# Performance work log

Measured on AMD Instinct MI355X. Metric: run time of the kernel, lower is better.

Reference implementation:

```python
import jax, jax.numpy as jnp
import numpy as np

B, C, H, W, R = 4, 128, 64, 256, 8  # batch, channels, height, width, window radius


def setup_inputs() -> dict:
    key = jax.random.key(0)
    k0, k1, k2, k3 = jax.random.split(key, 4)
    feature = jax.random.normal(k0, (B, C, H, W), dtype=jnp.float32)
    position = 0.02 * jax.random.normal(k1, (B, C, H, W), dtype=jnp.float32)
    # 1x1 conv weights (xavier-like scale), bias zeros as in nn.Conv2d default-ish
    Wq = jax.random.normal(k2, (C, C), dtype=jnp.float32) / np.float32(np.sqrt(C))
    Wk = jax.random.normal(k3, (C, C), dtype=jnp.float32) / np.float32(np.sqrt(C))
    bq = jnp.zeros((C,), dtype=jnp.float32)
    bk = jnp.zeros((C,), dtype=jnp.float32)
    return {"feature": feature, "position": position, "Wq": Wq, "bq": bq, "Wk": Wk, "bk": bk}


def reference(feature, position, Wq, bq, Wk, bk):
    # feature/position: [b, c, h, w]
    f = feature + position
    b, c, h, w = f.shape
    # 1x1 convs == channel matmuls
    q = jnp.einsum('oc,bchw->bohw', Wq, f) + bq[None, :, None, None]
    k = jnp.einsum('oc,bchw->bohw', Wk, f) + bk[None, :, None, None]
    r = R
    Kw = 2 * r + 1
    # pad along width, gather sliding windows: [b, c, h, w, Kw]
    kp = jnp.pad(k, ((0, 0), (0, 0), (0, 0), (r, r)))
    vp = jnp.pad(f, ((0, 0), (0, 0), (0, 0), (r, r)))
    idx = jnp.arange(w)[:, None] + jnp.arange(Kw)[None, :]  # [w, Kw]
    kwin = kp[:, :, :, idx]
    vwin = vp[:, :, :, idx]
    scale = jnp.asarray(np.sqrt(c), dtype=q.dtype)
    scores = jnp.einsum('bchw,bchwk->bhwk', q, kwin) / scale  # [b, h, w, Kw]
    attn = jax.nn.softmax(scores, axis=-1)
    out = jnp.einsum('bhwk,bchwk->bchw', attn, vwin)
    return out
```

## Files before the change

### kernel.cpp

```cpp
#include <hip/hip_runtime.h>
#include <hip/hip_bf16.h>
#include <math.h>

#define BB 4
#define CCH 128
#define HH 64
#define WW 256
#define RR 8
#define KWIN 17
#define TW 32
#define TWH 48
#define NTHREADS 256
#define PIT 136
#define PTP 56
#define MROWS 144

typedef __attribute__((ext_vector_type(8))) short short8;
typedef __attribute__((ext_vector_type(4))) short short4v;
typedef __attribute__((ext_vector_type(4))) float f32x4;

__device__ __forceinline__ short f2bf(float x) {
    union { __hip_bfloat16 b; short s; } u;
    u.b = __float2bfloat16(x);
    return u.s;
}

__global__ __launch_bounds__(256)
void prep_kernel(const float* __restrict__ Wq, const float* __restrict__ bq,
                 const float* __restrict__ Wk, short* __restrict__ Mp)
{
    const int t = threadIdx.x;
    const int r = blockIdx.x * 2 + (t >> 7);
    const int c = t & 127;
    float a0 = 0.f, a1 = 0.f, a2 = 0.f, a3 = 0.f;
    if (r < CCH) {
        #pragma unroll
        for (int j = 0; j < CCH; j += 4) {
            a0 = fmaf(Wq[(j + 0) * CCH + r], Wk[(j + 0) * CCH + c], a0);
            a1 = fmaf(Wq[(j + 1) * CCH + r], Wk[(j + 1) * CCH + c], a1);
            a2 = fmaf(Wq[(j + 2) * CCH + r], Wk[(j + 2) * CCH + c], a2);
            a3 = fmaf(Wq[(j + 3) * CCH + r], Wk[(j + 3) * CCH + c], a3);
        }
    } else if (r == CCH) {
        #pragma unroll
        for (int o = 0; o < CCH; o += 4) {
            a0 = fmaf(bq[o + 0], Wk[(o + 0) * CCH + c], a0);
            a1 = fmaf(bq[o + 1], Wk[(o + 1) * CCH + c], a1);
            a2 = fmaf(bq[o + 2], Wk[(o + 2) * CCH + c], a2);
            a3 = fmaf(bq[o + 3], Wk[(o + 3) * CCH + c], a3);
        }
    }
    Mp[r * CCH + c] = f2bf((a0 + a1) + (a2 + a3));
}

#define ST_IDX(r) (((r) >> 4) * 1088 + ((r) & 15) * 36)

__global__ __launch_bounds__(NTHREADS, 5)
void attn1d_fused(const float* __restrict__ feature,
                  const float* __restrict__ position,
                  const short* __restrict__ Mp,
                  float* __restrict__ out)
{
    __shared__ __align__(16) short fBt[TWH][PIT];
    __shared__ __align__(16) char  uB[TWH * PIT * 2];
    __shared__ __align__(16) short Pt[TW][PTP];
    __shared__ float ubias[TWH];
    short (*gT)[PIT]  = (short(*)[PIT])uB;
    float* Stp        = (float*)uB;

    const int t    = threadIdx.x;
    const int wid  = t >> 6;
    const int lane = t & 63;
    const int lrow = lane & 15;
    const int lgrp = lane >> 4;

    int blk = blockIdx.x;
    blk = (blk & 7) * 256 + (blk >> 3);
    const int wt = blk & 7;
    const int bh = blk >> 3;
    const int h  = bh & (HH - 1);
    const int b  = bh >> 6;
    const int w0 = wt * TW - RR;
    const int base = ((b * CCH) * HH + h) * WW;

    const int mrow = wid * 32;
    short8 Mf[2][4];
    #pragma unroll
    for (int mf = 0; mf < 2; ++mf)
        #pragma unroll
        for (int kk = 0; kk < 4; ++kk)
            Mf[mf][kk] = *(const short8*)(Mp + (mrow + mf * 16 + lrow) * CCH
                                             + kk * 32 + lgrp * 8);
    short8 Mf2[4];
    if (wid == 3) {
        #pragma unroll
        for (int kk = 0; kk < 4; ++kk)
            Mf2[kk] = *(const short8*)(Mp + (CCH + lrow) * CCH + kk * 32 + lgrp * 8);
    }

    #pragma unroll
    for (int i = 0; i < 6; ++i) {
        const int idx = i * NTHREADS + t;
        const int c  = idx / 12;
        const int wq = idx - c * 12;
        const int w  = w0 + wq * 4;
        float4 fv = {0.f, 0.f, 0.f, 0.f};
        if (w >= 0 && w < WW) {
            const int off = base + c * (HH * WW) + w;
            const float4 fa = *(const float4*)(feature + off);
            const float4 pa = *(const float4*)(position + off);
            fv.x = fa.x + pa.x; fv.y = fa.y + pa.y;
            fv.z = fa.z + pa.z; fv.w = fa.w + pa.w;
        }
        fBt[wq * 4 + 0][c] = f2bf(fv.x);
        fBt[wq * 4 + 1][c] = f2bf(fv.y);
        fBt[wq * 4 + 2][c] = f2bf(fv.z);
        fBt[wq * 4 + 3][c] = f2bf(fv.w);
    }
    __syncthreads();

    {
        f32x4 acc[2][3];
        #pragma unroll
        for (int mf = 0; mf < 2; ++mf)
            #pragma unroll
            for (int nf = 0; nf < 3; ++nf)
                acc[mf][nf] = (f32x4){0.f, 0.f, 0.f, 0.f};
        f32x4 acc2[3];
        #pragma unroll
        for (int nf = 0; nf < 3; ++nf) acc2[nf] = (f32x4){0.f, 0.f, 0.f, 0.f};

        #pragma unroll
        for (int kk = 0; kk < 4; ++kk) {
            short8 bfr[3];
            #pragma unroll
            for (int nf = 0; nf < 3; ++nf)
                bfr[nf] = *(const short8*)&fBt[nf * 16 + lrow][kk * 32 + lgrp * 8];
            #pragma unroll
            for (int mf = 0; mf < 2; ++mf)
                #pragma unroll
                for (int nf = 0; nf < 3; ++nf)
                    acc[mf][nf] = __builtin_amdgcn_mfma_f32_16x16x32_bf16(
                        Mf[mf][kk], bfr[nf], acc[mf][nf], 0, 0, 0);
            if (wid == 3) {
                #pragma unroll
                for (int nf = 0; nf < 3; ++nf)
                    acc2[nf] = __builtin_amdgcn_mfma_f32_16x16x32_bf16(
                        Mf2[kk], bfr[nf], acc2[nf], 0, 0, 0);
            }
        }

        #pragma unroll
        for (int mf = 0; mf < 2; ++mf)
            #pragma unroll
            for (int nf = 0; nf < 3; ++nf) {
                short4v s;
                #pragma unroll
                for (int reg = 0; reg < 4; ++reg)
                    s[reg] = f2bf(acc[mf][nf][reg]);
                *(short4v*)&gT[nf * 16 + lrow][mrow + mf * 16 + lgrp * 4] = s;
            }
        if (wid == 3 && lgrp == 0) {
            const float isc = 0.08838834764831845f;
            #pragma unroll
            for (int nf = 0; nf < 3; ++nf)
                ubias[nf * 16 + lrow] = acc2[nf][0] * isc;
        }
    }
    __syncthreads();

    if (wid < 3) {
        const int nf = wid;
        f32x4 s0 = {0.f,0.f,0.f,0.f}, s1 = {0.f,0.f,0.f,0.f};
        #pragma unroll
        for (int kk = 0; kk < 4; ++kk) {
            const short8 a0 = *(const short8*)&fBt[RR + lrow     ][kk * 32 + lgrp * 8];
            const short8 a1 = *(const short8*)&fBt[RR + 16 + lrow][kk * 32 + lgrp * 8];
            const short8 bb = *(const short8*)&gT[nf * 16 + lrow][kk * 32 + lgrp * 8];
            s0 = __builtin_amdgcn_mfma_f32_16x16x32_bf16(a0, bb, s0, 0, 0, 0);
            s1 = __builtin_amdgcn_mfma_f32_16x16x32_bf16(a1, bb, s1, 0, 0, 0);
        }
        const float isc = 0.08838834764831845f;
        const int sb = ST_IDX(nf * 16 + lrow);
        *(f32x4*)&Stp[sb + lgrp * 4]      = s0 * isc;
        *(f32x4*)&Stp[sb + 16 + lgrp * 4] = s1 * isc;
    } else {
        const short8 z = {0,0,0,0,0,0,0,0};
        short* p = &Pt[0][0];
        #pragma unroll
        for (int i = 0; i < 4; ++i) {
            const int q8 = i * 64 + lane;
            if (q8 < (TW * PTP) / 8) *(short8*)(p + q8 * 8) = z;
        }
    }
    __syncthreads();

    if (t < TW * 4) {
        const int w = t >> 2, g = t & 3;
        const int nt = (g == 0) ? 5 : 4;
        float sv[5];
        float mx = -3.0e38f;
        #pragma unroll
        for (int i = 0; i < 5; ++i) {
            if (i < nt) {
                const int j = (i == 4) ? 16 : (g + i * 4);
                const int r = w + j;
                sv[i] = Stp[ST_IDX(r) + w] + ubias[r];
                mx = fmaxf(mx, sv[i]);
            }
        }
        mx = fmaxf(mx, __shfl_xor(mx, 1, 4));
        mx = fmaxf(mx, __shfl_xor(mx, 2, 4));
        float sum = 0.f;
        #pragma unroll
        for (int i = 0; i < 5; ++i)
            if (i < nt) { sv[i] = __expf(sv[i] - mx); sum += sv[i]; }
        sum += __shfl_xor(sum, 1, 4);
        sum += __shfl_xor(sum, 2, 4);
        const float inv = 1.f / sum;
        #pragma unroll
        for (int i = 0; i < 5; ++i)
            if (i < nt) {
                const int j = (i == 4) ? 16 : (g + i * 4);
                Pt[w][w + j] = f2bf(sv[i] * inv);
            }
    }
    __syncthreads();

    {
        const int cb = wid * 32;
        const short8 z = {0,0,0,0,0,0,0,0};
        f32x4 d00 = {0.f,0.f,0.f,0.f}, d01 = d00, d10 = d00, d11 = d00;
        #pragma unroll
        for (int kk = 0; kk < 2; ++kk) {
            const int koff = kk * 32 + lgrp * 8;
            const bool live = (koff < TWH);
            short8 a0 = z, a1 = z, b0 = z, b1 = z;
            if (live) {
                #pragma unroll
                for (int j = 0; j < 8; ++j) {
                    a0[j] = fBt[koff + j][cb + lrow];
                    a1[j] = fBt[koff + j][cb + 16 + lrow];
                }
                b0 = *(const short8*)&Pt[lrow][koff];
                b1 = *(const short8*)&Pt[16 + lrow][koff];
            }
            d00 = __builtin_amdgcn_mfma_f32_16x16x32_bf16(a0, b0, d00, 0, 0, 0);
            d01 = __builtin_amdgcn_mfma_f32_16x16x32_bf16(a0, b1, d01, 0, 0, 0);
            d10 = __builtin_amdgcn_mfma_f32_16x16x32_bf16(a1, b0, d10, 0, 0, 0);
            d11 = __builtin_amdgcn_mfma_f32_16x16x32_bf16(a1, b1, d11, 0, 0, 0);
        }
        const int wbase = wt * TW;
        #pragma unroll
        for (int reg = 0; reg < 4; ++reg) {
            const int c0 = cb + lgrp * 4 + reg;
            out[base + c0 * (HH * WW)        + wbase + lrow]      = d00[reg];
            out[base + c0 * (HH * WW)        + wbase + 16 + lrow] = d01[reg];
            out[base + (c0 + 16) * (HH * WW) + wbase + lrow]      = d10[reg];
            out[base + (c0 + 16) * (HH * WW) + wbase + 16 + lrow] = d11[reg];
        }
    }
}

extern "C" void kernel_launch(void* const* d_in, const int* in_sizes, int n_in,
                              void* d_out, int out_size, void* d_ws, size_t ws_size,
                              hipStream_t stream) {
    const float* feature  = (const float*)d_in[0];
    const float* position = (const float*)d_in[1];
    const float* Wq = (const float*)d_in[2];
    const float* bq = (const float*)d_in[3];
    const float* Wk = (const float*)d_in[4];
    const float* bk = (const float*)d_in[5];
    (void)bk;
    float* out = (float*)d_out;
    short* Mp  = (short*)d_ws;

    prep_kernel<<<MROWS / 2, 256, 0, stream>>>(Wq, bq, Wk, Mp);
    const dim3 grid(BB * HH * (WW / TW));
    attn1d_fused<<<grid, NTHREADS, 0, stream>>>(feature, position, Mp, out);
}
```

Measured before the change: 43.36 us.

## Widen attention tile to 64 columns with 512 threads and channel-major value copy

Doubles the width tile from 32 to 64 output columns per block, so the 16-column halo is amortized over more outputs. Threads go from 256 to 512 and work is repartitioned across 8 waves. It also adds a channel-major bf16 copy of the features so the final P·V MFMA can read its A operand with vector loads instead of strided scalar gathers. In exchange, shared memory per block grows (a separate score/gT buffer plus the new fA array), which lowers occupancy, and there are half as many blocks.

```diff
diff --git a/kernel.cpp b/kernel.cpp
--- a/kernel.cpp
+++ b/kernel.cpp
@@ -8,11 +8,12 @@
 #define WW 256
 #define RR 8
 #define KWIN 17
-#define TW 32
-#define TWH 48
-#define NTHREADS 256
+#define TW 64
+#define TWH 80
+#define NTHREADS 512
 #define PIT 136
-#define PTP 56
+#define FAP 88
+#define PTP 88
 #define MROWS 144
 
 typedef __attribute__((ext_vector_type(8))) short short8;
@@ -53,20 +54,18 @@
     Mp[r * CCH + c] = f2bf((a0 + a1) + (a2 + a3));
 }
 
-#define ST_IDX(r) (((r) >> 4) * 1088 + ((r) & 15) * 36)
-
-__global__ __launch_bounds__(NTHREADS, 5)
+__global__ __launch_bounds__(NTHREADS, 4)
 void attn1d_fused(const float* __restrict__ feature,
                   const float* __restrict__ position,
                   const short* __restrict__ Mp,
                   float* __restrict__ out)
 {
     __shared__ __align__(16) short fBt[TWH][PIT];
-    __shared__ __align__(16) char  uB[TWH * PIT * 2];
-    __shared__ __align__(16) short Pt[TW][PTP];
+    __shared__ __align__(16) short gT [TWH][PIT];
+    __shared__ __align__(16) short fA [CCH][FAP];
+    __shared__ __align__(16) short Pt [TW ][PTP];
     __shared__ float ubias[TWH];
-    short (*gT)[PIT]  = (short(*)[PIT])uB;
-    float* Stp        = (float*)uB;
+    float* Stp = (float*)&gT[0][0];
 
     const int t    = threadIdx.x;
     const int wid  = t >> 6;
@@ -75,34 +74,31 @@
     const int lgrp = lane >> 4;
 
     int blk = blockIdx.x;
-    blk = (blk & 7) * 256 + (blk >> 3);
-    const int wt = blk & 7;
-    const int bh = blk >> 3;
+    blk = (blk & 7) * 128 + (blk >> 3);
+    const int wt = blk & 3;
+    const int bh = blk >> 2;
     const int h  = bh & (HH - 1);
     const int b  = bh >> 6;
     const int w0 = wt * TW - RR;
     const int base = ((b * CCH) * HH + h) * WW;
 
-    const int mrow = wid * 32;
-    short8 Mf[2][4];
+    const int mrow = wid * 16;
+    short8 Mf[4];
     #pragma unroll
-    for (int mf = 0; mf < 2; ++mf)
-        #pragma unroll
-        for (int kk = 0; kk < 4; ++kk)
-            Mf[mf][kk] = *(const short8*)(Mp + (mrow + mf * 16 + lrow) * CCH
-                                             + kk * 32 + lgrp * 8);
+    for (int kk = 0; kk < 4; ++kk)
+        Mf[kk] = *(const short8*)(Mp + (mrow + lrow) * CCH + kk * 32 + lgrp * 8);
     short8 Mf2[4];
-    if (wid == 3) {
+    if (wid == 7) {
         #pragma unroll
         for (int kk = 0; kk < 4; ++kk)
             Mf2[kk] = *(const short8*)(Mp + (CCH + lrow) * CCH + kk * 32 + lgrp * 8);
     }
 
     #pragma unroll
-    for (int i = 0; i < 6; ++i) {
+    for (int i = 0; i < 5; ++i) {
         const int idx = i * NTHREADS + t;
-        const int c  = idx / 12;
-        const int wq = idx - c * 12;
+        const int c  = idx / 20;
+        const int wq = idx - c * 20;
         const int w  = w0 + wq * 4;
         float4 fv = {0.f, 0.f, 0.f, 0.f};
         if (w >= 0 && w < WW) {
@@ -112,153 +108,151 @@
             fv.x = fa.x + pa.x; fv.y = fa.y + pa.y;
             fv.z = fa.z + pa.z; fv.w = fa.w + pa.w;
         }
-        fBt[wq * 4 + 0][c] = f2bf(fv.x);
-        fBt[wq * 4 + 1][c] = f2bf(fv.y);
-        fBt[wq * 4 + 2][c] = f2bf(fv.z);
-        fBt[wq * 4 + 3][c] = f2bf(fv.w);
+        short4v s4;
+        s4[0] = f2bf(fv.x); s4[1] = f2bf(fv.y); s4[2] = f2bf(fv.z); s4[3] = f2bf(fv.w);
+        *(short4v*)&fA[c][wq * 4] = s4;
+        fBt[wq * 4 + 0][c] = s4[0];
+        fBt[wq * 4 + 1][c] = s4[1];
+        fBt[wq * 4 + 2][c] = s4[2];
+        fBt[wq * 4 + 3][c] = s4[3];
     }
     __syncthreads();
 
     {
-        f32x4 acc[2][3];
-        #pragma unroll
-        for (int mf = 0; mf < 2; ++mf)
-            #pragma unroll
-            for (int nf = 0; nf < 3; ++nf)
-                acc[mf][nf] = (f32x4){0.f, 0.f, 0.f, 0.f};
-        f32x4 acc2[3];
-        #pragma unroll
-        for (int nf = 0; nf < 3; ++nf) acc2[nf] = (f32x4){0.f, 0.f, 0.f, 0.f};
+        f32x4 acc[5];
+        #pragma unroll
+        for (int nf = 0; nf < 5; ++nf) acc[nf] = (f32x4){0.f, 0.f, 0.f, 0.f};
+        f32x4 acc2[5];
+        #pragma unroll
+        for (int nf = 0; nf < 5; ++nf) acc2[nf] = (f32x4){0.f, 0.f, 0.f, 0.f};
 
         #pragma unroll
         for (int kk = 0; kk < 4; ++kk) {
-            short8 bfr[3];
-            #pragma unroll
-            for (int nf = 0; nf < 3; ++nf)
+            short8 bfr[5];
+            #pragma unroll
+            for (int nf = 0; nf < 5; ++nf)
                 bfr[nf] = *(const short8*)&fBt[nf * 16 + lrow][kk * 32 + lgrp * 8];
             #pragma unroll
-            for (int mf = 0; mf < 2; ++mf)
+            for (int nf = 0; nf < 5; ++nf)
+                acc[nf] = __builtin_amdgcn_mfma_f32_16x16x32_bf16(
+                    Mf[kk], bfr[nf], acc[nf], 0, 0, 0);
+            if (wid == 7) {
                 #pragma unroll
-                for (int nf = 0; nf < 3; ++nf)
-                    acc[mf][nf] = __builtin_amdgcn_mfma_f32_16x16x32_bf16(
-                        Mf[mf][kk], bfr[nf], acc[mf][nf], 0, 0, 0);
-            if (wid == 3) {
-                #pragma unroll
-                for (int nf = 0; nf < 3; ++nf)
+                for (int nf = 0; nf < 5; ++nf)
                     acc2[nf] = __builtin_amdgcn_mfma_f32_16x16x32_bf16(
                         Mf2[kk], bfr[nf], acc2[nf], 0, 0, 0);
             }
         }
 
         #pragma unroll
-        for (int mf = 0; mf < 2; ++mf)
-            #pragma unroll
-            for (int nf = 0; nf < 3; ++nf) {
-                short4v s;
-                #pragma unroll
-                for (int reg = 0; reg < 4; ++reg)
-                    s[reg] = f2bf(acc[mf][nf][reg]);
-                *(short4v*)&gT[nf * 16 + lrow][mrow + mf * 16 + lgrp * 4] = s;
-            }
-        if (wid == 3 && lgrp == 0) {
+        for (int nf = 0; nf < 5; ++nf) {
+            short4v s;
+            #pragma unroll
+            for (int reg = 0; reg < 4; ++reg)
+                s[reg] = f2bf(acc[nf][reg]);
+            *(short4v*)&gT[nf * 16 + lrow][mrow + lgrp * 4] = s;
+        }
+        if (wid == 7 && lgrp == 0) {
             const float isc = 0.08838834764831845f;
             #pragma unroll
-            for (int nf = 0; nf < 3; ++nf)
+            for (int nf = 0; nf < 5; ++nf)
                 ubias[nf * 16 + lrow] = acc2[nf][0] * isc;
         }
     }
     __syncthreads();
 
-    if (wid < 3) {
-        const int nf = wid;
-        f32x4 s0 = {0.f,0.f,0.f,0.f}, s1 = {0.f,0.f,0.f,0.f};
+    if (wid < 5) {
+        const int nb = wid;
+        f32x4 s[4];
+        #pragma unroll
+        for (int na = 0; na < 4; ++na) s[na] = (f32x4){0.f, 0.f, 0.f, 0.f};
         #pragma unroll
         for (int kk = 0; kk < 4; ++kk) {
-            const short8 a0 = *(const short8*)&fBt[RR + lrow     ][kk * 32 + lgrp * 8];
-            const short8 a1 = *(const short8*)&fBt[RR + 16 + lrow][kk * 32 + lgrp * 8];
-            const short8 bb = *(const short8*)&gT[nf * 16 + lrow][kk * 32 + lgrp * 8];
-            s0 = __builtin_amdgcn_mfma_f32_16x16x32_bf16(a0, bb, s0, 0, 0, 0);
-            s1 = __builtin_amdgcn_mfma_f32_16x16x32_bf16(a1, bb, s1, 0, 0, 0);
+            const short8 bb = *(const short8*)&gT[nb * 16 + lrow][kk * 32 + lgrp * 8];
+            #pragma unroll
+            for (int na = 0; na < 4; ++na) {
+                const short8 aa = *(const short8*)
+                    &fBt[RR + na * 16 + lrow][kk * 32 + lgrp * 8];
+                s[na] = __builtin_amdgcn_mfma_f32_16x16x32_bf16(aa, bb, s[na], 0, 0, 0);
+            }
         }
         const float isc = 0.08838834764831845f;
-        const int sb = ST_IDX(nf * 16 + lrow);
-        *(f32x4*)&Stp[sb + lgrp * 4]      = s0 * isc;
-        *(f32x4*)&Stp[sb + 16 + lgrp * 4] = s1 * isc;
+        #pragma unroll
+        for (int na = 0; na < 4; ++na)
+            *(f32x4*)&Stp[nb * 1088 + lrow * 68 + na * 16 + lgrp * 4] = s[na] * isc;
     } else {
         const short8 z = {0,0,0,0,0,0,0,0};
+        const int id = (wid - 5) * 64 + lane;
         short* p = &Pt[0][0];
         #pragma unroll
         for (int i = 0; i < 4; ++i) {
-            const int q8 = i * 64 + lane;
+            const int q8 = i * 192 + id;
             if (q8 < (TW * PTP) / 8) *(short8*)(p + q8 * 8) = z;
         }
     }
     __syncthreads();
 
-    if (t < TW * 4) {
-        const int w = t >> 2, g = t & 3;
-        const int nt = (g == 0) ? 5 : 4;
-        float sv[5];
+    {
+        const int w = t >> 3, g = t & 7;
+        const int nt = (g == 0) ? 3 : 2;
+        float sv[3];
         float mx = -3.0e38f;
         #pragma unroll
-        for (int i = 0; i < 5; ++i) {
+        for (int i = 0; i < 3; ++i) {
             if (i < nt) {
-                const int j = (i == 4) ? 16 : (g + i * 4);
+                const int j = (i == 2) ? 16 : (g + i * 8);
                 const int r = w + j;
-                sv[i] = Stp[ST_IDX(r) + w] + ubias[r];
+                sv[i] = Stp[(r >> 4) * 1088 + (r & 15) * 68 + w] + ubias[r];
                 mx = fmaxf(mx, sv[i]);
             }
         }
-        mx = fmaxf(mx, __shfl_xor(mx, 1, 4));
-        mx = fmaxf(mx, __shfl_xor(mx, 2, 4));
+        mx = fmaxf(mx, __shfl_xor(mx, 1, 8));
+        mx = fmaxf(mx, __shfl_xor(mx, 2, 8));
+        mx = fmaxf(mx, __shfl_xor(mx, 4, 8));
         float sum = 0.f;
         #pragma unroll
-        for (int i = 0; i < 5; ++i)
+        for (int i = 0; i < 3; ++i)
             if (i < nt) { sv[i] = __expf(sv[i] - mx); sum += sv[i]; }
-        sum += __shfl_xor(sum, 1, 4);
-        sum += __shfl_xor(sum, 2, 4);
+        sum += __shfl_xor(sum, 1, 8);
+        sum += __shfl_xor(sum, 2, 8);
+        sum += __shfl_xor(sum, 4, 8);
         const float inv = 1.f / sum;
         #pragma unroll
-        for (int i = 0; i < 5; ++i)
+        for (int i = 0; i < 3; ++i)
             if (i < nt) {
-                const int j = (i == 4) ? 16 : (g + i * 4);
+                const int j = (i == 2) ? 16 : (g + i * 8);
                 Pt[w][w + j] = f2bf(sv[i] * inv);
             }
     }
     __syncthreads();
 
     {
-        const int cb = wid * 32;
+        const int cb = wid * 16;
         const short8 z = {0,0,0,0,0,0,0,0};
-        f32x4 d00 = {0.f,0.f,0.f,0.f}, d01 = d00, d10 = d00, d11 = d00;
-        #pragma unroll
-        for (int kk = 0; kk < 2; ++kk) {
+        f32x4 d[4];
+        #pragma unroll
+        for (int nf = 0; nf < 4; ++nf) d[nf] = (f32x4){0.f, 0.f, 0.f, 0.f};
+        #pragma unroll
+        for (int kk = 0; kk < 3; ++kk) {
             const int koff = kk * 32 + lgrp * 8;
             const bool live = (koff < TWH);
-            short8 a0 = z, a1 = z, b0 = z, b1 = z;
-            if (live) {
-                #pragma unroll
-                for (int j = 0; j < 8; ++j) {
-                    a0[j] = fBt[koff + j][cb + lrow];
-                    a1[j] = fBt[koff + j][cb + 16 + lrow];
-                }
-                b0 = *(const short8*)&Pt[lrow][koff];
-                b1 = *(const short8*)&Pt[16 + lrow][koff];
-            }
-            d00 = __builtin_amdgcn_mfma_f32_16x16x32_bf16(a0, b0, d00, 0, 0, 0);
-            d01 = __builtin_amdgcn_mfma_f32_16x16x32_bf16(a0, b1, d01, 0, 0, 0);
-            d10 = __builtin_amdgcn_mfma_f32_16x16x32_bf16(a1, b0, d10, 0, 0, 0);
-            d11 = __builtin_amdgcn_mfma_f32_16x16x32_bf16(a1, b1, d11, 0, 0, 0);
+            short8 aa = z;
+            if (live) aa = *(const short8*)&fA[cb + lrow][koff];
+            #pragma unroll
+            for (int nf = 0; nf < 4; ++nf) {
+                short8 bb = z;
+                if (live) bb = *(const short8*)&Pt[nf * 16 + lrow][koff];
+                d[nf] = __builtin_amdgcn_mfma_f32_16x16x32_bf16(aa, bb, d[nf], 0, 0, 0);
+            }
         }
         const int wbase = wt * TW;
         #pragma unroll
-        for (int reg = 0; reg < 4; ++reg) {
-            const int c0 = cb + lgrp * 4 + reg;
-            out[base + c0 * (HH * WW)        + wbase + lrow]      = d00[reg];
-            out[base + c0 * (HH * WW)        + wbase + 16 + lrow] = d01[reg];
-            out[base + (c0 + 16) * (HH * WW) + wbase + lrow]      = d10[reg];
-            out[base + (c0 + 16) * (HH * WW) + wbase + 16 + lrow] = d11[reg];
-        }
+        for (int nf = 0; nf < 4; ++nf)
+            #pragma unroll
+            for (int reg = 0; reg < 4; ++reg) {
+                const int c0 = cb + lgrp * 4 + reg;
+                out[base + c0 * (HH * WW) + wbase + nf * 16 + lrow] = d[nf][reg];
+            }
     }
 }
 
```

After: 36.34 us. 1.19x faster.
